# Kernel tuning notes

Measured on AMD Instinct MI355X. Metric: run time of the kernel, lower is better.

The kernel has to match this reference:

```python
import jax, jax.numpy as jnp
import numpy as np

TEMPERATURE = 0.5
HEAD_DIM = 64
NUM_HEADS = 4

N_NODES = 50000
N_EDGES = 800000
DIM = 256


def setup_inputs() -> dict:
    key = jax.random.key(0)
    ks = jax.random.split(key, 7)
    h = jax.random.normal(ks[0], (N_NODES, DIM), dtype=jnp.float32)
    src = jax.random.randint(ks[1], (N_EDGES,), 0, N_NODES)
    dst = jax.random.randint(ks[2], (N_EDGES,), 0, N_NODES)
    attn_q = jax.random.normal(ks[3], (DIM, NUM_HEADS * HEAD_DIM), dtype=jnp.float32) * 0.02
    attn_k = jax.random.normal(ks[4], (DIM, NUM_HEADS * HEAD_DIM), dtype=jnp.float32) * 0.02
    W = jax.random.normal(ks[5], (DIM, DIM), dtype=jnp.float32) * (1.0 / np.sqrt(DIM))
    b = jnp.zeros((DIM,), dtype=jnp.float32)
    return {"h": h, "src": src, "dst": dst, "attn_q": attn_q, "attn_k": attn_k, "W": W, "b": b}


def _edge_softmax_by_dst(a, dst, n_nodes):
    # softmax over incoming edges of each destination node (DGL edge_softmax)
    m = jax.ops.segment_max(a, dst, num_segments=n_nodes)
    e = jnp.exp(a - m[dst])
    s = jax.ops.segment_sum(e, dst, num_segments=n_nodes)
    return e / s[dst]


def reference(h, src, dst, attn_q, attn_k, W, b):
    n = h.shape[0]
    v = h @ W.T + b                         # iv Linear: [N, D]
    q = h @ attn_q                          # [N, H*64]
    k = h @ attn_k                          # [N, H*64]
    # per-edge score: mean over heads then over head_dim == mean over all H*64,
    # preceded by /8 -> dot(q_src, k_dst) / (8 * H * 64)
    scale = 1.0 / (8.0 * NUM_HEADS * HEAD_DIM)
    a = jnp.einsum('ed,ed->e', q[src], k[dst]) * scale   # [E]
    # global standardization over all edges (std unbiased=False)
    m = a.mean()
    s = jnp.sqrt(((a - m) ** 2).mean())
    a = (a - m) / s / TEMPERATURE
    a = _edge_softmax_by_dst(a, dst, n)     # [E]
    # message passing: sum_{e: dst(e)=i} a_e * v[src(e)]
    out = jax.ops.segment_sum(v[src] * a[:, None], dst, num_segments=n)  # [N, D]
    return out, a
```

## Files before the change

kernel.cpp:

```cpp
#include <hip/hip_runtime.h>
#include <math.h>

#define DIM 256
#define NQKV 768
#define STAT_BLOCKS 2048

typedef float  f32x4 __attribute__((ext_vector_type(4)));
typedef short  bs8   __attribute__((ext_vector_type(8)));

__device__ __forceinline__ ushort f2bf(float f) {
    unsigned int u = __float_as_uint(f);
    u += 0x7fffu + ((u >> 16) & 1u);
    return (ushort)(u >> 16);
}
__device__ __forceinline__ float bf2f(ushort u) {
    return __uint_as_float(((unsigned int)u) << 16);
}
__device__ __forceinline__ float dotu4(uint4 a, uint4 b) {
    float s;
    s  = bf2f((ushort)a.x) * bf2f((ushort)b.x) + bf2f((ushort)(a.x >> 16)) * bf2f((ushort)(b.x >> 16));
    s += bf2f((ushort)a.y) * bf2f((ushort)b.y) + bf2f((ushort)(a.y >> 16)) * bf2f((ushort)(b.y >> 16));
    s += bf2f((ushort)a.z) * bf2f((ushort)b.z) + bf2f((ushort)(a.z >> 16)) * bf2f((ushort)(b.z >> 16));
    s += bf2f((ushort)a.w) * bf2f((ushort)b.w) + bf2f((ushort)(a.w >> 16)) * bf2f((ushort)(b.w >> 16));
    return s;
}

#define MFMA16(c, a, b) \
    asm("s_nop 1\n\tv_mfma_f32_16x16x32_bf16 %0, %1, %2, %0" : "+v"(c) : "v"(a), "v"(b))

#define GLOAD_LDS16(g, l) __builtin_amdgcn_global_load_lds( \
    (const __attribute__((address_space(1))) unsigned int*)(g), \
    (__attribute__((address_space(3))) unsigned int*)(l), 16, 0, 0)

__global__ __launch_bounds__(256) void conv_h(
    const float* __restrict__ h, ushort* __restrict__ h_bf, int total8)
{
    const int idx = blockIdx.x * 256 + threadIdx.x;
    if (idx >= total8) return;
    const float4* hp = (const float4*)(h + (size_t)idx * 8);
    float4 a = hp[0], b = hp[1];
    uint4 o;
    o.x = (unsigned)f2bf(a.x) | ((unsigned)f2bf(a.y) << 16);
    o.y = (unsigned)f2bf(a.z) | ((unsigned)f2bf(a.w) << 16);
    o.z = (unsigned)f2bf(b.x) | ((unsigned)f2bf(b.y) << 16);
    o.w = (unsigned)f2bf(b.z) | ((unsigned)f2bf(b.w) << 16);
    *(uint4*)(h_bf + (size_t)idx * 8) = o;
}

__global__ __launch_bounds__(256) void build_bt(
    const float* __restrict__ attn_q, const float* __restrict__ attn_k,
    const float* __restrict__ W, ushort* __restrict__ bt)
{
    const int n = blockIdx.x;
    const int k = threadIdx.x;
    float val;
    if (n < 256)      val = attn_q[(size_t)k * 256 + n];
    else if (n < 512) val = attn_k[(size_t)k * 256 + (n - 256)];
    else              val = W[(size_t)(n - 512) * 256 + k];
    bt[(size_t)n * 256 + k] = f2bf(val);
}

__global__ __launch_bounds__(256) void gemm_qkv_mfma(
    const ushort* __restrict__ h_bf, const ushort* __restrict__ bt,
    const float* __restrict__ bias, ushort* __restrict__ qkv, int M)
{
    __shared__ __align__(16) ushort As[128 * 32];
    __shared__ __align__(16) ushort Bs[128 * 32];

    const int bm = blockIdx.x * 128;
    const int bn = blockIdx.y * 128;
    const int t    = threadIdx.x;
    const int lane = t & 63;
    const int wid  = t >> 6;
    const int wm   = wid >> 1;
    const int wn   = wid & 1;
    const int fr   = lane & 15;

    const int srow0 = wid * 32 + (lane >> 2);
    const int srow1 = srow0 + 16;
    const int g0 = (lane & 3) ^ (srow0 & 3);
    const int g1 = (lane & 3) ^ (srow1 & 3);
    const int ga0 = min(bm + srow0, M - 1);
    const int ga1 = min(bm + srow1, M - 1);
    const int rchunk = ((lane >> 4) ^ (fr & 3)) * 8;

    f32x4 acc[4][4];
    #pragma unroll
    for (int i = 0; i < 4; ++i)
        #pragma unroll
        for (int j = 0; j < 4; ++j)
            acc[i][j] = (f32x4){0.f, 0.f, 0.f, 0.f};

    for (int k0 = 0; k0 < DIM; k0 += 32) {
        GLOAD_LDS16(h_bf + (size_t)ga0 * 256 + k0 + g0 * 8, As + (wid * 32) * 32);
        GLOAD_LDS16(h_bf + (size_t)ga1 * 256 + k0 + g1 * 8, As + (wid * 32 + 16) * 32);
        GLOAD_LDS16(bt + (size_t)(bn + srow0) * 256 + k0 + g0 * 8, Bs + (wid * 32) * 32);
        GLOAD_LDS16(bt + (size_t)(bn + srow1) * 256 + k0 + g1 * 8, Bs + (wid * 32 + 16) * 32);
        asm volatile("s_waitcnt vmcnt(0)" ::: "memory");
        __syncthreads();

        bs8 af[4], bf_[4];
        #pragma unroll
        for (int f = 0; f < 4; ++f) {
            af[f]  = *(const bs8*)(As + (wm * 64 + f * 16 + fr) * 32 + rchunk);
            bf_[f] = *(const bs8*)(Bs + (wn * 64 + f * 16 + fr) * 32 + rchunk);
        }
        #pragma unroll
        for (int fm = 0; fm < 4; ++fm)
            #pragma unroll
            for (int fn = 0; fn < 4; ++fn)
                MFMA16(acc[fm][fn], af[fm], bf_[fn]);

        __syncthreads();
    }

    asm volatile("s_nop 7\n\ts_nop 7\n\ts_nop 7" ::: );

    #pragma unroll
    for (int fm = 0; fm < 4; ++fm) {
        const int rowbase = bm + wm * 64 + fm * 16 + (lane >> 4) * 4;
        #pragma unroll
        for (int fn = 0; fn < 4; ++fn) {
            const int col = bn + wn * 64 + fn * 16 + fr;
            float bv = (col >= 512) ? bias[col - 512] : 0.f;
            #pragma unroll
            for (int r = 0; r < 4; ++r) {
                const int row = rowbase + r;
                if (row < M)
                    qkv[(size_t)row * NQKV + col] = f2bf(acc[fm][fn][r] + bv);
            }
        }
    }
}

__global__ __launch_bounds__(256) void deg_count(
    const int* __restrict__ dst, int* __restrict__ deg, int E)
{
    const int e = blockIdx.x * 256 + threadIdx.x;
    if (e < E) atomicAdd(&deg[dst[e]], 1);
}

__global__ __launch_bounds__(1024) void scan_rowptr(
    const int* __restrict__ deg, int* __restrict__ row_ptr, int N)
{
    const int tid  = threadIdx.x;
    const int lane = tid & 63;
    const int wv   = tid >> 6;

    if (tid == 0) row_ptr[0] = 0;

    __shared__ int woff[17];
    __shared__ int carryS;
    if (tid == 0) carryS = 0;
    __syncthreads();

    for (int base = 0; base < N; base += 4096) {
        int x[4], pre[4];
        int run = 0;
        #pragma unroll
        for (int j = 0; j < 4; ++j) {
            const int i = base + tid * 4 + j;
            const int v = (i < N) ? deg[i] : 0;
            pre[j] = run; x[j] = v; run += v;
        }
        int incl = run;
        #pragma unroll
        for (int off = 1; off < 64; off <<= 1) {
            int y = __shfl_up(incl, off);
            if (lane >= off) incl += y;
        }
        const int wex = incl - run;
        if (lane == 63) woff[wv] = incl;
        __syncthreads();
        if (wv == 0) {
            int wtot = (lane < 16) ? woff[lane] : 0;
            int winc = wtot;
            #pragma unroll
            for (int off = 1; off < 16; off <<= 1) {
                int y = __shfl_up(winc, off);
                if (lane >= off) winc += y;
            }
            if (lane < 16) woff[lane] = winc - wtot;
            if (lane == 15) woff[16] = winc;
        }
        __syncthreads();
        const int basev = carryS + woff[wv] + wex;
        #pragma unroll
        for (int j = 0; j < 4; ++j) {
            const int i = base + tid * 4 + j;
            if (i < N) row_ptr[i + 1] = basev + pre[j] + x[j];
        }
        __syncthreads();
        if (tid == 0) carryS += woff[16];
        __syncthreads();
    }
}

__global__ __launch_bounds__(256) void scatter_edges(
    const int* __restrict__ src, const int* __restrict__ dst,
    const int* __restrict__ row_ptr, int* __restrict__ cursor,
    int4* __restrict__ edata, int E)
{
    const int e = blockIdx.x * 256 + threadIdx.x;
    if (e < E) {
        const int d = dst[e];
        const int pos = row_ptr[d] + atomicAdd(&cursor[d], 1);
        edata[pos] = make_int4(src[e], d, e, 0);
    }
}

__global__ __launch_bounds__(256) void edge_dot_csr(
    const ushort* __restrict__ qkv, const int4* __restrict__ edata,
    float* __restrict__ a_rawc, double* __restrict__ partials, int E)
{
    const int lane = threadIdx.x & 63;
    const int wid  = threadIdx.x >> 6;
    const int lq   = lane & 31;
    const int hh   = lane >> 5;
    const int w    = blockIdx.x * 4 + wid;
    const int nw   = gridDim.x * 4;
    const int chunk = (E + nw - 1) / nw;
    const int p0 = min(E, w * chunk);
    const int p1 = min(E, p0 + chunk);

    double lsum = 0.0, lsum2 = 0.0;
    int p = p0;

    for (; p + 8 <= p1; p += 8) {
        const int4 ed0 = edata[p     + hh];
        const int4 ed1 = edata[p + 2 + hh];
        const int4 ed2 = edata[p + 4 + hh];
        const int4 ed3 = edata[p + 6 + hh];
        uint4 q0 = *(const uint4*)(qkv + (size_t)ed0.x * NQKV + lq * 8);
        uint4 q1 = *(const uint4*)(qkv + (size_t)ed1.x * NQKV + lq * 8);
        uint4 q2 = *(const uint4*)(qkv + (size_t)ed2.x * NQKV + lq * 8);
        uint4 q3 = *(const uint4*)(qkv + (size_t)ed3.x * NQKV + lq * 8);
        uint4 k0 = *(const uint4*)(qkv + (size_t)ed0.y * NQKV + 256 + lq * 8);
        uint4 k1 = *(const uint4*)(qkv + (size_t)ed1.y * NQKV + 256 + lq * 8);
        uint4 k2 = *(const uint4*)(qkv + (size_t)ed2.y * NQKV + 256 + lq * 8);
        uint4 k3 = *(const uint4*)(qkv + (size_t)ed3.y * NQKV + 256 + lq * 8);
        float d0 = dotu4(q0, k0);
        float d1 = dotu4(q1, k1);
        float d2 = dotu4(q2, k2);
        float d3 = dotu4(q3, k3);
        #pragma unroll
        for (int off = 16; off; off >>= 1) {
            d0 += __shfl_xor(d0, off);
            d1 += __shfl_xor(d1, off);
            d2 += __shfl_xor(d2, off);
            d3 += __shfl_xor(d3, off);
        }
        if (lq == 0) {
            a_rawc[p     + hh] = d0;
            a_rawc[p + 2 + hh] = d1;
            a_rawc[p + 4 + hh] = d2;
            a_rawc[p + 6 + hh] = d3;
            lsum  += (double)d0 + (double)d1 + (double)d2 + (double)d3;
            lsum2 += (double)d0 * d0 + (double)d1 * d1
                   + (double)d2 * d2 + (double)d3 * d3;
        }
    }
    for (; p + 2 <= p1; p += 2) {
        const int4 ed0 = edata[p + hh];
        uint4 q0 = *(const uint4*)(qkv + (size_t)ed0.x * NQKV + lq * 8);
        uint4 k0 = *(const uint4*)(qkv + (size_t)ed0.y * NQKV + 256 + lq * 8);
        float d0 = dotu4(q0, k0);
        #pragma unroll
        for (int off = 16; off; off >>= 1) d0 += __shfl_xor(d0, off);
        if (lq == 0) {
            a_rawc[p + hh] = d0;
            lsum  += (double)d0;
            lsum2 += (double)d0 * d0;
        }
    }
    if (p < p1) {
        const int4 ed0 = edata[p];
        uint4 q0 = *(const uint4*)(qkv + (size_t)ed0.x * NQKV + lq * 8);
        uint4 k0 = *(const uint4*)(qkv + (size_t)ed0.y * NQKV + 256 + lq * 8);
        float d0 = dotu4(q0, k0);
        #pragma unroll
        for (int off = 16; off; off >>= 1) d0 += __shfl_xor(d0, off);
        if (lane == 0) {
            a_rawc[p] = d0;
            lsum  += (double)d0;
            lsum2 += (double)d0 * d0;
        }
    }

    lsum  += __shfl_xor(lsum, 32);
    lsum2 += __shfl_xor(lsum2, 32);

    __shared__ double bsum[4], bsum2[4];
    if (lane == 0) { bsum[wid] = lsum; bsum2[wid] = lsum2; }
    __syncthreads();
    if (threadIdx.x == 0) {
        partials[blockIdx.x]             = bsum[0] + bsum[1] + bsum[2] + bsum[3];
        partials[gridDim.x + blockIdx.x] = bsum2[0] + bsum2[1] + bsum2[2] + bsum2[3];
    }
}

__global__ __launch_bounds__(256) void finalize_coef(
    const double* __restrict__ partials, float* __restrict__ coef, int E)
{
    __shared__ double red[256];
    const int tid = threadIdx.x;
    double s1 = 0.0, s2 = 0.0;
    for (int i = tid; i < STAT_BLOCKS; i += 256) {
        s1 += partials[i];
        s2 += partials[STAT_BLOCKS + i];
    }
    red[tid] = s1;
    __syncthreads();
    for (int off = 128; off; off >>= 1) {
        if (tid < off) red[tid] += red[tid + off];
        __syncthreads();
    }
    const double tot1 = red[0];
    __syncthreads();
    red[tid] = s2;
    __syncthreads();
    for (int off = 128; off; off >>= 1) {
        if (tid < off) red[tid] += red[tid + off];
        __syncthreads();
    }
    if (tid == 0) {
        const double mean = tot1 / (double)E;
        const double var  = red[0] / (double)E - mean * mean;
        coef[0] = (float)mean;
        coef[1] = (float)(1.0 / (sqrt(var) * 0.5));
    }
}

__global__ __launch_bounds__(256) void agg_fused(
    const ushort* __restrict__ qkv, const float* __restrict__ a_rawc,
    const int4* __restrict__ edata, const int* __restrict__ row_ptr,
    const float* __restrict__ coef,
    float* __restrict__ out, float* __restrict__ a_out, int N)
{
    const int lane = threadIdx.x & 63;
    const int wv   = threadIdx.x >> 6;
    const int node = blockIdx.x * 4 + wv;
    if (node >= N) return;

    const int s   = row_ptr[node];
    const int deg = row_ptr[node + 1] - s;
    const float mean = coef[0];
    const float mul  = coef[1];

    __shared__ float wbuf_s[4][128];
    __shared__ int   sbuf_s[4][128];
    float* wbuf = wbuf_s[wv];
    int*   sbuf = sbuf_s[wv];

    float lsum = 0.f;
    for (int j = lane; j < deg; j += 64)
        lsum += __expf((a_rawc[s + j] - mean) * mul);
    #pragma unroll
    for (int off = 32; off; off >>= 1) lsum += __shfl_xor(lsum, off);
    const float rcp = 1.0f / lsum;

    float4 acc = make_float4(0.f, 0.f, 0.f, 0.f);
    for (int b0 = 0; b0 < deg; b0 += 128) {
        const int bc = min(128, deg - b0);
        for (int j = lane; j < bc; j += 64) {
            const int4 ed = edata[s + b0 + j];
            const float wgt = __expf((a_rawc[s + b0 + j] - mean) * mul) * rcp;
            wbuf[j] = wgt;
            sbuf[j] = ed.x;
            a_out[ed.z] = wgt;
        }
        asm volatile("s_waitcnt lgkmcnt(0)" ::: "memory");
        __builtin_amdgcn_sched_barrier(0);

        int j = 0;
        for (; j + 4 <= bc; j += 4) {
            const float w0 = wbuf[j],     w1 = wbuf[j + 1];
            const float w2 = wbuf[j + 2], w3 = wbuf[j + 3];
            const int   s0 = sbuf[j],     s1 = sbuf[j + 1];
            const int   s2 = sbuf[j + 2], s3 = sbuf[j + 3];
            ushort4 v0 = *(const ushort4*)(qkv + (size_t)s0 * NQKV + 512 + lane * 4);
            ushort4 v1 = *(const ushort4*)(qkv + (size_t)s1 * NQKV + 512 + lane * 4);
            ushort4 v2 = *(const ushort4*)(qkv + (size_t)s2 * NQKV + 512 + lane * 4);
            ushort4 v3 = *(const ushort4*)(qkv + (size_t)s3 * NQKV + 512 + lane * 4);
            acc.x += w0 * bf2f(v0.x) + w1 * bf2f(v1.x) + w2 * bf2f(v2.x) + w3 * bf2f(v3.x);
            acc.y += w0 * bf2f(v0.y) + w1 * bf2f(v1.y) + w2 * bf2f(v2.y) + w3 * bf2f(v3.y);
            acc.z += w0 * bf2f(v0.z) + w1 * bf2f(v1.z) + w2 * bf2f(v2.z) + w3 * bf2f(v3.z);
            acc.w += w0 * bf2f(v0.w) + w1 * bf2f(v1.w) + w2 * bf2f(v2.w) + w3 * bf2f(v3.w);
        }
        for (; j < bc; ++j) {
            const float w0 = wbuf[j];
            const int   s0 = sbuf[j];
            ushort4 v0 = *(const ushort4*)(qkv + (size_t)s0 * NQKV + 512 + lane * 4);
            acc.x += w0 * bf2f(v0.x);
            acc.y += w0 * bf2f(v0.y);
            acc.z += w0 * bf2f(v0.z);
            acc.w += w0 * bf2f(v0.w);
        }
    }

    *(float4*)&out[(size_t)node * DIM + lane * 4] = acc;
}

extern "C" void kernel_launch(void* const* d_in, const int* in_sizes, int n_in,
                              void* d_out, int out_size, void* d_ws, size_t ws_size,
                              hipStream_t stream)
{
    const float* h      = (const float*)d_in[0];
    const int*   src    = (const int*)d_in[1];
    const int*   dst    = (const int*)d_in[2];
    const float* attn_q = (const float*)d_in[3];
    const float* attn_k = (const float*)d_in[4];
    const float* W      = (const float*)d_in[5];
    const float* bias   = (const float*)d_in[6];

    const int N = in_sizes[0] / DIM;
    const int E = in_sizes[1];

    float* out   = (float*)d_out;
    float* a_out = out + (size_t)N * DIM;

    char* ws = (char*)d_ws;
    ushort* h_bf  = (ushort*)ws;
    int4*   edata = (int4*)ws;
    ws += (size_t)N * DIM * 2;
    ushort* qkv   = (ushort*)ws; ws += (size_t)N * NQKV * 2;
    ushort* bt    = (ushort*)ws; ws += (size_t)NQKV * DIM * 2;
    float* a_rawc = (float*)ws;  ws += (size_t)E * 4;
    int* deg      = (int*)ws;    ws += (size_t)N * 4;
    int* cursor   = (int*)ws;    ws += (size_t)N * 4;
    double* partials = (double*)ws; ws += (size_t)STAT_BLOCKS * 2 * 8;
    float* coef   = (float*)ws;  ws += 8;
    int* row_ptr  = (int*)ws;    ws += (size_t)(N + 1) * 4;

    hipMemsetAsync(deg,    0, (size_t)N * 4, stream);
    hipMemsetAsync(cursor, 0, (size_t)N * 4, stream);

    const int total8 = N * DIM / 8;
    conv_h<<<(total8 + 255) / 256, 256, 0, stream>>>(h, h_bf, total8);
    build_bt<<<NQKV, 256, 0, stream>>>(attn_q, attn_k, W, bt);

    dim3 gg((N + 127) / 128, NQKV / 128);
    gemm_qkv_mfma<<<gg, 256, 0, stream>>>(h_bf, bt, bias, qkv, N);

    deg_count<<<(E + 255) / 256, 256, 0, stream>>>(dst, deg, E);
    scan_rowptr<<<1, 1024, 0, stream>>>(deg, row_ptr, N);
    scatter_edges<<<(E + 255) / 256, 256, 0, stream>>>(src, dst, row_ptr, cursor, edata, E);
    edge_dot_csr<<<STAT_BLOCKS, 256, 0, stream>>>(qkv, edata, a_rawc, partials, E);
    finalize_coef<<<1, 256, 0, stream>>>(partials, coef, E);
    agg_fused<<<(N + 3) / 4, 256, 0, stream>>>(qkv, a_rawc, edata, row_ptr, coef, out, a_out, N);
}
```

Before: 422.3 us.

## Fuse prep kernels, overlap edge scatter with GEMM, and drop finalize launch

Combines the h conversion, weight transpose and degree count into one launch, and runs the CSR scatter as extra blocks of the QKV GEMM grid. The cursor now starts from the scanned row pointer. The coefficient finalize moves into edge_dot_csr through a last-block atomic counter. Edge data is split from int4 records into separate src, dst and original-index arrays, and the aggregation inner loop is unrolled to 8 gathers. The aim is to cut launch count and serialization between small kernels, at the cost of extra workspace and of mixing heterogeneous work in one grid.

```diff
diff --git a/kernel.cpp b/kernel.cpp
--- a/kernel.cpp
+++ b/kernel.cpp
@@ -32,43 +32,124 @@
     (const __attribute__((address_space(1))) unsigned int*)(g), \
     (__attribute__((address_space(3))) unsigned int*)(l), 16, 0, 0)
 
-__global__ __launch_bounds__(256) void conv_h(
-    const float* __restrict__ h, ushort* __restrict__ h_bf, int total8)
-{
-    const int idx = blockIdx.x * 256 + threadIdx.x;
-    if (idx >= total8) return;
-    const float4* hp = (const float4*)(h + (size_t)idx * 8);
-    float4 a = hp[0], b = hp[1];
-    uint4 o;
-    o.x = (unsigned)f2bf(a.x) | ((unsigned)f2bf(a.y) << 16);
-    o.y = (unsigned)f2bf(a.z) | ((unsigned)f2bf(a.w) << 16);
-    o.z = (unsigned)f2bf(b.x) | ((unsigned)f2bf(b.y) << 16);
-    o.w = (unsigned)f2bf(b.z) | ((unsigned)f2bf(b.w) << 16);
-    *(uint4*)(h_bf + (size_t)idx * 8) = o;
-}
-
-__global__ __launch_bounds__(256) void build_bt(
+__global__ __launch_bounds__(256) void prep(
+    const float* __restrict__ h, ushort* __restrict__ h_bf, int total8, int nbConv,
     const float* __restrict__ attn_q, const float* __restrict__ attn_k,
-    const float* __restrict__ W, ushort* __restrict__ bt)
-{
-    const int n = blockIdx.x;
-    const int k = threadIdx.x;
-    float val;
-    if (n < 256)      val = attn_q[(size_t)k * 256 + n];
-    else if (n < 512) val = attn_k[(size_t)k * 256 + (n - 256)];
-    else              val = W[(size_t)(n - 512) * 256 + k];
-    bt[(size_t)n * 256 + k] = f2bf(val);
-}
-
-__global__ __launch_bounds__(256) void gemm_qkv_mfma(
+    const float* __restrict__ W, ushort* __restrict__ bt,
+    const int* __restrict__ dst, int* __restrict__ deg, int E)
+{
+    const int bx = blockIdx.x;
+    if (bx < nbConv) {
+        const int idx = bx * 256 + threadIdx.x;
+        if (idx >= total8) return;
+        const float4* hp = (const float4*)(h + (size_t)idx * 8);
+        float4 a = hp[0], b = hp[1];
+        uint4 o;
+        o.x = (unsigned)f2bf(a.x) | ((unsigned)f2bf(a.y) << 16);
+        o.y = (unsigned)f2bf(a.z) | ((unsigned)f2bf(a.w) << 16);
+        o.z = (unsigned)f2bf(b.x) | ((unsigned)f2bf(b.y) << 16);
+        o.w = (unsigned)f2bf(b.z) | ((unsigned)f2bf(b.w) << 16);
+        *(uint4*)(h_bf + (size_t)idx * 8) = o;
+    } else if (bx < nbConv + NQKV) {
+        const int n = bx - nbConv;
+        const int k = threadIdx.x;
+        float val;
+        if (n < 256)      val = attn_q[(size_t)k * 256 + n];
+        else if (n < 512) val = attn_k[(size_t)k * 256 + (n - 256)];
+        else              val = W[(size_t)(n - 512) * 256 + k];
+        bt[(size_t)n * 256 + k] = f2bf(val);
+    } else {
+        const int e = (bx - nbConv - NQKV) * 256 + threadIdx.x;
+        if (e < E) atomicAdd(&deg[dst[e]], 1);
+    }
+}
+
+__global__ __launch_bounds__(1024) void scan_rowptr(
+    const int* __restrict__ deg, int* __restrict__ row_ptr,
+    int* __restrict__ cursor, int N)
+{
+    const int tid  = threadIdx.x;
+    const int lane = tid & 63;
+    const int wv   = tid >> 6;
+
+    if (tid == 0) { row_ptr[0] = 0; cursor[0] = 0; }
+
+    __shared__ int woff[17];
+    __shared__ int carryS;
+    if (tid == 0) carryS = 0;
+    __syncthreads();
+
+    for (int base = 0; base < N; base += 4096) {
+        int x[4], pre[4];
+        int run = 0;
+        #pragma unroll
+        for (int j = 0; j < 4; ++j) {
+            const int i = base + tid * 4 + j;
+            const int v = (i < N) ? deg[i] : 0;
+            pre[j] = run; x[j] = v; run += v;
+        }
+        int incl = run;
+        #pragma unroll
+        for (int off = 1; off < 64; off <<= 1) {
+            int y = __shfl_up(incl, off);
+            if (lane >= off) incl += y;
+        }
+        const int wex = incl - run;
+        if (lane == 63) woff[wv] = incl;
+        __syncthreads();
+        if (wv == 0) {
+            int wtot = (lane < 16) ? woff[lane] : 0;
+            int winc = wtot;
+            #pragma unroll
+            for (int off = 1; off < 16; off <<= 1) {
+                int y = __shfl_up(winc, off);
+                if (lane >= off) winc += y;
+            }
+            if (lane < 16) woff[lane] = winc - wtot;
+            if (lane == 15) woff[16] = winc;
+        }
+        __syncthreads();
+        const int basev = carryS + woff[wv] + wex;
+        #pragma unroll
+        for (int j = 0; j < 4; ++j) {
+            const int i = base + tid * 4 + j;
+            if (i < N) {
+                const int v = basev + pre[j] + x[j];
+                row_ptr[i + 1] = v;
+                cursor[i + 1]  = v;
+            }
+        }
+        __syncthreads();
+        if (tid == 0) carryS += woff[16];
+        __syncthreads();
+    }
+}
+
+__global__ __launch_bounds__(256) void gemm_scatter(
     const ushort* __restrict__ h_bf, const ushort* __restrict__ bt,
-    const float* __restrict__ bias, ushort* __restrict__ qkv, int M)
+    const float* __restrict__ bias, ushort* __restrict__ qkv, int M, int nbGemm,
+    const int* __restrict__ src, const int* __restrict__ dst,
+    int* __restrict__ cursor,
+    int* __restrict__ srcc, int* __restrict__ dstc, int* __restrict__ orige, int E)
 {
     __shared__ __align__(16) ushort As[128 * 32];
     __shared__ __align__(16) ushort Bs[128 * 32];
 
-    const int bm = blockIdx.x * 128;
-    const int bn = blockIdx.y * 128;
+    const int bx = blockIdx.x;
+    if (bx >= nbGemm) {
+        const int e = (bx - nbGemm) * 256 + threadIdx.x;
+        if (e < E) {
+            const int d = dst[e];
+            const int pos = atomicAdd(&cursor[d], 1);
+            srcc[pos]  = src[e];
+            dstc[pos]  = d;
+            orige[pos] = e;
+        }
+        return;
+    }
+
+    const int bm = (bx / 6) * 128;
+    const int bn = (bx % 6) * 128;
     const int t    = threadIdx.x;
     const int lane = t & 63;
     const int wid  = t >> 6;
@@ -133,85 +214,11 @@
     }
 }
 
-__global__ __launch_bounds__(256) void deg_count(
-    const int* __restrict__ dst, int* __restrict__ deg, int E)
-{
-    const int e = blockIdx.x * 256 + threadIdx.x;
-    if (e < E) atomicAdd(&deg[dst[e]], 1);
-}
-
-__global__ __launch_bounds__(1024) void scan_rowptr(
-    const int* __restrict__ deg, int* __restrict__ row_ptr, int N)
-{
-    const int tid  = threadIdx.x;
-    const int lane = tid & 63;
-    const int wv   = tid >> 6;
-
-    if (tid == 0) row_ptr[0] = 0;
-
-    __shared__ int woff[17];
-    __shared__ int carryS;
-    if (tid == 0) carryS = 0;
-    __syncthreads();
-
-    for (int base = 0; base < N; base += 4096) {
-        int x[4], pre[4];
-        int run = 0;
-        #pragma unroll
-        for (int j = 0; j < 4; ++j) {
-            const int i = base + tid * 4 + j;
-            const int v = (i < N) ? deg[i] : 0;
-            pre[j] = run; x[j] = v; run += v;
-        }
-        int incl = run;
-        #pragma unroll
-        for (int off = 1; off < 64; off <<= 1) {
-            int y = __shfl_up(incl, off);
-            if (lane >= off) incl += y;
-        }
-        const int wex = incl - run;
-        if (lane == 63) woff[wv] = incl;
-        __syncthreads();
-        if (wv == 0) {
-            int wtot = (lane < 16) ? woff[lane] : 0;
-            int winc = wtot;
-            #pragma unroll
-            for (int off = 1; off < 16; off <<= 1) {
-                int y = __shfl_up(winc, off);
-                if (lane >= off) winc += y;
-            }
-            if (lane < 16) woff[lane] = winc - wtot;
-            if (lane == 15) woff[16] = winc;
-        }
-        __syncthreads();
-        const int basev = carryS + woff[wv] + wex;
-        #pragma unroll
-        for (int j = 0; j < 4; ++j) {
-            const int i = base + tid * 4 + j;
-            if (i < N) row_ptr[i + 1] = basev + pre[j] + x[j];
-        }
-        __syncthreads();
-        if (tid == 0) carryS += woff[16];
-        __syncthreads();
-    }
-}
-
-__global__ __launch_bounds__(256) void scatter_edges(
-    const int* __restrict__ src, const int* __restrict__ dst,
-    const int* __restrict__ row_ptr, int* __restrict__ cursor,
-    int4* __restrict__ edata, int E)
-{
-    const int e = blockIdx.x * 256 + threadIdx.x;
-    if (e < E) {
-        const int d = dst[e];
-        const int pos = row_ptr[d] + atomicAdd(&cursor[d], 1);
-        edata[pos] = make_int4(src[e], d, e, 0);
-    }
-}
-
 __global__ __launch_bounds__(256) void edge_dot_csr(
-    const ushort* __restrict__ qkv, const int4* __restrict__ edata,
-    float* __restrict__ a_rawc, double* __restrict__ partials, int E)
+    const ushort* __restrict__ qkv,
+    const int* __restrict__ srcc, const int* __restrict__ dstc,
+    float* __restrict__ a_rawc, double* __restrict__ partials,
+    int* __restrict__ done, float* __restrict__ coef, int E)
 {
     const int lane = threadIdx.x & 63;
     const int wid  = threadIdx.x >> 6;
@@ -227,18 +234,18 @@
     int p = p0;
 
     for (; p + 8 <= p1; p += 8) {
-        const int4 ed0 = edata[p     + hh];
-        const int4 ed1 = edata[p + 2 + hh];
-        const int4 ed2 = edata[p + 4 + hh];
-        const int4 ed3 = edata[p + 6 + hh];
-        uint4 q0 = *(const uint4*)(qkv + (size_t)ed0.x * NQKV + lq * 8);
-        uint4 q1 = *(const uint4*)(qkv + (size_t)ed1.x * NQKV + lq * 8);
-        uint4 q2 = *(const uint4*)(qkv + (size_t)ed2.x * NQKV + lq * 8);
-        uint4 q3 = *(const uint4*)(qkv + (size_t)ed3.x * NQKV + lq * 8);
-        uint4 k0 = *(const uint4*)(qkv + (size_t)ed0.y * NQKV + 256 + lq * 8);
-        uint4 k1 = *(const uint4*)(qkv + (size_t)ed1.y * NQKV + 256 + lq * 8);
-        uint4 k2 = *(const uint4*)(qkv + (size_t)ed2.y * NQKV + 256 + lq * 8);
-        uint4 k3 = *(const uint4*)(qkv + (size_t)ed3.y * NQKV + 256 + lq * 8);
+        const int s0 = srcc[p     + hh], d0i = dstc[p     + hh];
+        const int s1 = srcc[p + 2 + hh], d1i = dstc[p + 2 + hh];
+        const int s2 = srcc[p + 4 + hh], d2i = dstc[p + 4 + hh];
+        const int s3 = srcc[p + 6 + hh], d3i = dstc[p + 6 + hh];
+        uint4 q0 = *(const uint4*)(qkv + (size_t)s0 * NQKV + lq * 8);
+        uint4 q1 = *(const uint4*)(qkv + (size_t)s1 * NQKV + lq * 8);
+        uint4 q2 = *(const uint4*)(qkv + (size_t)s2 * NQKV + lq * 8);
+        uint4 q3 = *(const uint4*)(qkv + (size_t)s3 * NQKV + lq * 8);
+        uint4 k0 = *(const uint4*)(qkv + (size_t)d0i * NQKV + 256 + lq * 8);
+        uint4 k1 = *(const uint4*)(qkv + (size_t)d1i * NQKV + 256 + lq * 8);
+        uint4 k2 = *(const uint4*)(qkv + (size_t)d2i * NQKV + 256 + lq * 8);
+        uint4 k3 = *(const uint4*)(qkv + (size_t)d3i * NQKV + 256 + lq * 8);
         float d0 = dotu4(q0, k0);
         float d1 = dotu4(q1, k1);
         float d2 = dotu4(q2, k2);
@@ -261,9 +268,9 @@
         }
     }
     for (; p + 2 <= p1; p += 2) {
-        const int4 ed0 = edata[p + hh];
-        uint4 q0 = *(const uint4*)(qkv + (size_t)ed0.x * NQKV + lq * 8);
-        uint4 k0 = *(const uint4*)(qkv + (size_t)ed0.y * NQKV + 256 + lq * 8);
+        const int s0 = srcc[p + hh], d0i = dstc[p + hh];
+        uint4 q0 = *(const uint4*)(qkv + (size_t)s0 * NQKV + lq * 8);
+        uint4 k0 = *(const uint4*)(qkv + (size_t)d0i * NQKV + 256 + lq * 8);
         float d0 = dotu4(q0, k0);
         #pragma unroll
         for (int off = 16; off; off >>= 1) d0 += __shfl_xor(d0, off);
@@ -274,9 +281,9 @@
         }
     }
     if (p < p1) {
-        const int4 ed0 = edata[p];
-        uint4 q0 = *(const uint4*)(qkv + (size_t)ed0.x * NQKV + lq * 8);
-        uint4 k0 = *(const uint4*)(qkv + (size_t)ed0.y * NQKV + 256 + lq * 8);
+        const int s0 = srcc[p], d0i = dstc[p];
+        uint4 q0 = *(const uint4*)(qkv + (size_t)s0 * NQKV + lq * 8);
+        uint4 k0 = *(const uint4*)(qkv + (size_t)d0i * NQKV + 256 + lq * 8);
         float d0 = dotu4(q0, k0);
         #pragma unroll
         for (int off = 16; off; off >>= 1) d0 += __shfl_xor(d0, off);
@@ -297,33 +304,36 @@
         partials[blockIdx.x]             = bsum[0] + bsum[1] + bsum[2] + bsum[3];
         partials[gridDim.x + blockIdx.x] = bsum2[0] + bsum2[1] + bsum2[2] + bsum2[3];
     }
-}
-
-__global__ __launch_bounds__(256) void finalize_coef(
-    const double* __restrict__ partials, float* __restrict__ coef, int E)
-{
+
+    __threadfence();
+    __shared__ int lastFlag;
+    if (threadIdx.x == 0)
+        lastFlag = (atomicAdd(done, 1) == (int)gridDim.x - 1);
+    __syncthreads();
+    if (!lastFlag) return;
+    __threadfence();
+
     __shared__ double red[256];
-    const int tid = threadIdx.x;
     double s1 = 0.0, s2 = 0.0;
-    for (int i = tid; i < STAT_BLOCKS; i += 256) {
+    for (int i = threadIdx.x; i < STAT_BLOCKS; i += 256) {
         s1 += partials[i];
         s2 += partials[STAT_BLOCKS + i];
     }
-    red[tid] = s1;
+    red[threadIdx.x] = s1;
     __syncthreads();
     for (int off = 128; off; off >>= 1) {
-        if (tid < off) red[tid] += red[tid + off];
+        if (threadIdx.x < off) red[threadIdx.x] += red[threadIdx.x + off];
         __syncthreads();
     }
     const double tot1 = red[0];
     __syncthreads();
-    red[tid] = s2;
+    red[threadIdx.x] = s2;
     __syncthreads();
     for (int off = 128; off; off >>= 1) {
-        if (tid < off) red[tid] += red[tid + off];
-        __syncthreads();
-    }
-    if (tid == 0) {
+        if (threadIdx.x < off) red[threadIdx.x] += red[threadIdx.x + off];
+        __syncthreads();
+    }
+    if (threadIdx.x == 0) {
         const double mean = tot1 / (double)E;
         const double var  = red[0] / (double)E - mean * mean;
         coef[0] = (float)mean;
@@ -333,8 +343,8 @@
 
 __global__ __launch_bounds__(256) void agg_fused(
     const ushort* __restrict__ qkv, const float* __restrict__ a_rawc,
-    const int4* __restrict__ edata, const int* __restrict__ row_ptr,
-    const float* __restrict__ coef,
+    const int* __restrict__ srcc, const int* __restrict__ orige,
+    const int* __restrict__ row_ptr, const float* __restrict__ coef,
     float* __restrict__ out, float* __restrict__ a_out, int N)
 {
     const int lane = threadIdx.x & 63;
@@ -363,29 +373,30 @@
     for (int b0 = 0; b0 < deg; b0 += 128) {
         const int bc = min(128, deg - b0);
         for (int j = lane; j < bc; j += 64) {
-            const int4 ed = edata[s + b0 + j];
             const float wgt = __expf((a_rawc[s + b0 + j] - mean) * mul) * rcp;
             wbuf[j] = wgt;
-            sbuf[j] = ed.x;
-            a_out[ed.z] = wgt;
+            sbuf[j] = srcc[s + b0 + j];
+            a_out[orige[s + b0 + j]] = wgt;
         }
         asm volatile("s_waitcnt lgkmcnt(0)" ::: "memory");
         __builtin_amdgcn_sched_barrier(0);
 
         int j = 0;
-        for (; j + 4 <= bc; j += 4) {
-            const float w0 = wbuf[j],     w1 = wbuf[j + 1];
-            const float w2 = wbuf[j + 2], w3 = wbuf[j + 3];
-            const int   s0 = sbuf[j],     s1 = sbuf[j + 1];
-            const int   s2 = sbuf[j + 2], s3 = sbuf[j + 3];
-            ushort4 v0 = *(const ushort4*)(qkv + (size_t)s0 * NQKV + 512 + lane * 4);
-            ushort4 v1 = *(const ushort4*)(qkv + (size_t)s1 * NQKV + 512 + lane * 4);
-            ushort4 v2 = *(const ushort4*)(qkv + (size_t)s2 * NQKV + 512 + lane * 4);
-            ushort4 v3 = *(const ushort4*)(qkv + (size_t)s3 * NQKV + 512 + lane * 4);
-            acc.x += w0 * bf2f(v0.x) + w1 * bf2f(v1.x) + w2 * bf2f(v2.x) + w3 * bf2f(v3.x);
-            acc.y += w0 * bf2f(v0.y) + w1 * bf2f(v1.y) + w2 * bf2f(v2.y) + w3 * bf2f(v3.y);
-            acc.z += w0 * bf2f(v0.z) + w1 * bf2f(v1.z) + w2 * bf2f(v2.z) + w3 * bf2f(v3.z);
-            acc.w += w0 * bf2f(v0.w) + w1 * bf2f(v1.w) + w2 * bf2f(v2.w) + w3 * bf2f(v3.w);
+        for (; j + 8 <= bc; j += 8) {
+            float wv8[8]; int si8[8];
+            #pragma unroll
+            for (int u = 0; u < 8; ++u) { wv8[u] = wbuf[j + u]; si8[u] = sbuf[j + u]; }
+            ushort4 vv[8];
+            #pragma unroll
+            for (int u = 0; u < 8; ++u)
+                vv[u] = *(const ushort4*)(qkv + (size_t)si8[u] * NQKV + 512 + lane * 4);
+            #pragma unroll
+            for (int u = 0; u < 8; ++u) {
+                acc.x += wv8[u] * bf2f(vv[u].x);
+                acc.y += wv8[u] * bf2f(vv[u].y);
+                acc.z += wv8[u] * bf2f(vv[u].z);
+                acc.w += wv8[u] * bf2f(vv[u].w);
+            }
         }
         for (; j < bc; ++j) {
             const float w0 = wbuf[j];
@@ -420,32 +431,37 @@
     float* a_out = out + (size_t)N * DIM;
 
     char* ws = (char*)d_ws;
-    ushort* h_bf  = (ushort*)ws;
-    int4*   edata = (int4*)ws;
-    ws += (size_t)N * DIM * 2;
+    ushort* h_bf  = (ushort*)ws; ws += (size_t)N * DIM * 2;
     ushort* qkv   = (ushort*)ws; ws += (size_t)N * NQKV * 2;
     ushort* bt    = (ushort*)ws; ws += (size_t)NQKV * DIM * 2;
     float* a_rawc = (float*)ws;  ws += (size_t)E * 4;
+    int* srcc     = (int*)ws;    ws += (size_t)E * 4;
+    int* dstc     = (int*)ws;    ws += (size_t)E * 4;
+    int* orige    = (int*)ws;    ws += (size_t)E * 4;
     int* deg      = (int*)ws;    ws += (size_t)N * 4;
-    int* cursor   = (int*)ws;    ws += (size_t)N * 4;
+    int* done     = (int*)ws;    ws += 64;
+    int* cursor   = (int*)ws;    ws += (size_t)(N + 1) * 4;
     double* partials = (double*)ws; ws += (size_t)STAT_BLOCKS * 2 * 8;
-    float* coef   = (float*)ws;  ws += 8;
+    float* coef   = (float*)ws;  ws += 64;
     int* row_ptr  = (int*)ws;    ws += (size_t)(N + 1) * 4;
 
-    hipMemsetAsync(deg,    0, (size_t)N * 4, stream);
-    hipMemsetAsync(cursor, 0, (size_t)N * 4, stream);
+    hipMemsetAsync(deg, 0, (size_t)N * 4 + 64, stream);
 
     const int total8 = N * DIM / 8;
-    conv_h<<<(total8 + 255) / 256, 256, 0, stream>>>(h, h_bf, total8);
-    build_bt<<<NQKV, 256, 0, stream>>>(attn_q, attn_k, W, bt);
-
-    dim3 gg((N + 127) / 128, NQKV / 128);
-    gemm_qkv_mfma<<<gg, 256, 0, stream>>>(h_bf, bt, bias, qkv, N);
-
-    deg_count<<<(E + 255) / 256, 256, 0, stream>>>(dst, deg, E);
-    scan_rowptr<<<1, 1024, 0, stream>>>(deg, row_ptr, N);
-    scatter_edges<<<(E + 255) / 256, 256, 0, stream>>>(src, dst, row_ptr, cursor, edata, E);
-    edge_dot_csr<<<STAT_BLOCKS, 256, 0, stream>>>(qkv, edata, a_rawc, partials, E);
-    finalize_coef<<<1, 256, 0, stream>>>(partials, coef, E);
-    agg_fused<<<(N + 3) / 4, 256, 0, stream>>>(qkv, a_rawc, edata, row_ptr, coef, out, a_out, N);
-}
+    const int nbConv = (total8 + 255) / 256;
+    const int nbDeg  = (E + 255) / 256;
+    prep<<<nbConv + NQKV + nbDeg, 256, 0, stream>>>(
+        h, h_bf, total8, nbConv, attn_q, attn_k, W, bt, dst, deg, E);
+
+    scan_rowptr<<<1, 1024, 0, stream>>>(deg, row_ptr, cursor, N);
+
+    const int nbGemm = ((N + 127) / 128) * 6;
+    gemm_scatter<<<nbGemm + nbDeg, 256, 0, stream>>>(
+        h_bf, bt, bias, qkv, N, nbGemm, src, dst, cursor, srcc, dstc, orige, E);
+
+    edge_dot_csr<<<STAT_BLOCKS, 256, 0, stream>>>(
+        qkv, srcc, dstc, a_rawc, partials, done, coef, E);
+
+    agg_fused<<<(N + 3) / 4, 256, 0, stream>>>(
+        qkv, a_rawc, srcc, orige, row_ptr, coef, out, a_out, N);
+}
```

New measurement: 705.0 us. 66.9% more time.
